# Performance work log

Hardware: AMD Instinct MI355X
Metric: run time of the kernel (lower is better)

The kernel has to match this reference:

```python
import jax, jax.numpy as jnp
import numpy as np

TEMPERATURE = 10.0
EPS = 1e-12  # torch F.normalize eps


def setup_inputs() -> dict:
    key = jax.random.key(0)
    k1, k2 = jax.random.split(key)
    B, D = 8192, 1024
    text_embeddings = jax.random.normal(k1, (B, D), dtype=jnp.float32)
    image_embeddings = jax.random.normal(k2, (B, D), dtype=jnp.float32)
    bias = jnp.zeros((1,), dtype=jnp.float32)
    return {
        "text_embeddings": text_embeddings,
        "image_embeddings": image_embeddings,
        "bias": bias,
    }


def _normalize(x):
    # matches torch F.normalize(p=2, dim=1): x / max(||x||, eps)
    norm = jnp.linalg.norm(x, axis=-1, keepdims=True)
    return x / jnp.maximum(norm, EPS)


def reference(text_embeddings, image_embeddings, bias):
    B = text_embeddings.shape[0]
    img_n = _normalize(image_embeddings)   # [B, D]
    txt_n = _normalize(text_embeddings)    # [B, D]
    # similarity[i, j] = <img_i, txt_j>
    sim = jnp.einsum('id,jd->ij', img_n, txt_n)          # [B, B]
    logits = sim * (-TEMPERATURE) + bias[0]
    labels = 2.0 * jnp.eye(B, dtype=logits.dtype) - 1.0   # +1 diag, -1 off-diag
    # loss_ij = log(1/(1+exp(label*logit))) = -softplus(label*logit)
    total_loss = -jnp.sum(jax.nn.softplus(labels * logits))
    return -(total_loss / B)
```

## Files before the change

### kernel.cpp

```cpp
#include <hip/hip_runtime.h>
#include <stdint.h>
#include <stddef.h>

#define NROWS 8192
#define DIM   1024
#define RB    512
#define TEMP  10.0f

#define BM 256
#define BN 256
#define BK 128

typedef __attribute__((ext_vector_type(8))) int i32x8;
typedef __attribute__((ext_vector_type(16))) float floatx16;

__device__ __forceinline__ void load16_lds(const unsigned char* g, unsigned char* l) {
    __builtin_amdgcn_global_load_lds(
        (__attribute__((address_space(1))) void*)(g),
        (__attribute__((address_space(3))) void*)(l),
        16, 0, 0);
}

__device__ __forceinline__ unsigned fp4q(float x) {
    float a = fabsf(x);
    a = fminf(a, 6.0f);
    unsigned c = (unsigned)(a >= 0.25f) + (unsigned)(a >= 0.75f)
               + (unsigned)(a >= 1.25f) + (unsigned)(a >= 1.75f)
               + (unsigned)(a >= 2.5f)  + (unsigned)(a >= 3.5f)
               + (unsigned)(a >= 5.0f);
    return c | ((__float_as_uint(x) >> 28) & 8u);
}

__device__ __forceinline__ i32x8 op8(int4 lo) {
    union { i32x8 v; int4 q[2]; } u;
    u.q[0] = lo;
    u.q[1] = make_int4(0, 0, 0, 0);
    return u.v;
}

__global__ __launch_bounds__(256) void normalize_kernel(
    const float* __restrict__ img, const float* __restrict__ txt,
    unsigned char* __restrict__ imgq, unsigned char* __restrict__ txtq,
    float* __restrict__ out)
{
    const int gw = blockIdx.x * 4 + (threadIdx.x >> 6);
    const int lane = threadIdx.x & 63;
    const float* src;
    unsigned char* dst;
    if (gw < NROWS) {
        src = img + (size_t)gw * DIM;
        dst = imgq + (size_t)gw * RB;
    } else {
        src = txt + (size_t)(gw - NROWS) * DIM;
        dst = txtq + (size_t)(gw - NROWS) * RB;
    }
    float4 v[4];
    float ss = 0.f;
#pragma unroll
    for (int c = 0; c < 4; c++) {
        v[c] = ((const float4*)src)[lane + 64 * c];
        ss += v[c].x * v[c].x + v[c].y * v[c].y + v[c].z * v[c].z + v[c].w * v[c].w;
    }
#pragma unroll
    for (int off = 32; off; off >>= 1) ss += __shfl_xor(ss, off);
    const float scale = 32.0f / fmaxf(sqrtf(ss), 1e-12f);
#pragma unroll
    for (int c = 0; c < 4; c++) {
        unsigned p = fp4q(v[c].x * scale)
                   | (fp4q(v[c].y * scale) << 4)
                   | (fp4q(v[c].z * scale) << 8)
                   | (fp4q(v[c].w * scale) << 12);
        ((unsigned short*)dst)[lane + 64 * c] = (unsigned short)p;
    }
    if (gw == 0 && lane == 0) out[0] = 0.f;
}

__global__ __launch_bounds__(512, 1) void simloss_kernel(
    const unsigned char* __restrict__ An,
    const unsigned char* __restrict__ Bn,
    const float* __restrict__ bias,
    float* __restrict__ out)
{
    __shared__ unsigned char As[2][BM * 64];
    __shared__ unsigned char Bs[2][BN * 64];
    __shared__ float red[24];

    const int t = threadIdx.x;
    const int lane = t & 63;
    const int wave = t >> 6;

    const int bid = blockIdx.x;
    const int blockN = (bid & 7) + 8 * ((bid >> 3) & 3);
    const int blockM = bid >> 5;

    int rowS[2], chS[2];
#pragma unroll
    for (int i = 0; i < 2; i++) {
        const int S = t + i * 512;
        const int pair = S >> 3, s7 = S & 7;
        rowS[i] = 2 * pair + (s7 & 1);
        chS[i] = ((s7 >> 1) ^ pair) & 3;
    }
    const unsigned char* gA0 = An + (size_t)(blockM * BM + rowS[0]) * RB + chS[0] * 16;
    const unsigned char* gA1 = An + (size_t)(blockM * BM + rowS[1]) * RB + chS[1] * 16;
    const unsigned char* gB0 = Bn + (size_t)(blockN * BN + rowS[0]) * RB + chS[0] * 16;
    const unsigned char* gB1 = Bn + (size_t)(blockN * BN + rowS[1]) * RB + chS[1] * 16;

    const int waveM = (wave >> 2) * 128;
    const int waveN = (wave & 3) * 64;
    const int fr = lane & 31;
    const int fh = lane >> 5;
    const int qk = (fr >> 1) & 3;
    const int po = 128 * (fr >> 1) + 16 * (fr & 1);
    const int offc0 = 32 * ((fh ^ qk) & 3);

    floatx16 acc[4][2];
#pragma unroll
    for (int mi = 0; mi < 4; mi++)
#pragma unroll
        for (int ni = 0; ni < 2; ni++)
            acc[mi][ni] = (floatx16)(0.f);

    load16_lds(gA0, &As[0][t * 16]);
    load16_lds(gA1, &As[0][t * 16 + 8192]);
    load16_lds(gB0, &Bs[0][t * 16]);
    load16_lds(gB1, &Bs[0][t * 16 + 8192]);

#pragma unroll
    for (int it = 0; it < DIM / BK; it++) {
        const int cur = it & 1;
        __syncthreads();
        if (it < DIM / BK - 1) {
            const int kb = (it + 1) * 64;
            load16_lds(gA0 + kb, &As[cur ^ 1][t * 16]);
            load16_lds(gA1 + kb, &As[cur ^ 1][t * 16 + 8192]);
            load16_lds(gB0 + kb, &Bs[cur ^ 1][t * 16]);
            load16_lds(gB1 + kb, &Bs[cur ^ 1][t * 16 + 8192]);
        }

        asm volatile("s_setprio 1");
#pragma unroll
        for (int ks = 0; ks < 2; ks++) {
            const int offc = offc0 ^ (ks << 6);
            int4 b[2];
#pragma unroll
            for (int ni = 0; ni < 2; ni++)
                b[ni] = *(const int4*)&Bs[cur][64 * (waveN + 32 * ni) + po + offc];
#pragma unroll
            for (int mi = 0; mi < 4; mi++) {
                int4 a = *(const int4*)&As[cur][64 * (waveM + 32 * mi) + po + offc];
#pragma unroll
                for (int ni = 0; ni < 2; ni++)
                    acc[mi][ni] = __builtin_amdgcn_mfma_scale_f32_32x32x64_f8f6f4(
                        op8(a), op8(b[ni]), acc[mi][ni],
                        4, 4,
                        0, 0x7f7f7f7f,
                        0, 0x7f7f7f7f);
            }
        }
        asm volatile("s_setprio 0");
    }

    const float bv = bias[0];
    const float c1 = -TEMP * 1.4426950408889634f / 1024.0f;
    const float c0 = bv * 1.4426950408889634f;
    float accP = 0.f, accQ = 0.f, accD = 0.f;
    const int gi0 = blockM * BM + waveM + 4 * fh;
    const int gj0 = blockN * BN + waveN + fr;
#pragma unroll
    for (int mi = 0; mi < 4; mi++) {
#pragma unroll
        for (int ni = 0; ni < 2; ni++) {
#pragma unroll
            for (int reg = 0; reg < 16; reg++) {
                float s = acc[mi][ni][reg];
                float w = fmaf(s, c1, c0);
                float e2 = __builtin_amdgcn_exp2f(-fabsf(w));
                accP += __builtin_amdgcn_logf(1.0f + e2);
                accP = fmaf(0.5f, fabsf(w), accP);
                accQ += s;
            }
        }
    }
    const bool diagblk = (blockN == blockM);
    if (diagblk) {
#pragma unroll
        for (int mi = 0; mi < 4; mi++)
#pragma unroll
            for (int ni = 0; ni < 2; ni++)
#pragma unroll
                for (int reg = 0; reg < 16; reg++) {
                    int ig = gi0 + mi * 32 + (reg & 3) + 8 * (reg >> 2);
                    int jg = gj0 + ni * 32;
                    if (ig == jg) accD += acc[mi][ni][reg];
                }
    }
#pragma unroll
    for (int off = 32; off; off >>= 1) {
        accP += __shfl_xor(accP, off);
        accQ += __shfl_xor(accQ, off);
        accD += __shfl_xor(accD, off);
    }
    if (lane == 0) {
        red[wave * 3 + 0] = accP;
        red[wave * 3 + 1] = accQ;
        red[wave * 3 + 2] = accD;
    }
    __syncthreads();
    if (t == 0) {
        float P = 0.f, Q = 0.f, D = 0.f;
#pragma unroll
        for (int w = 0; w < 8; w++) {
            P += red[w * 3 + 0];
            Q += red[w * 3 + 1];
            D += red[w * 3 + 2];
        }
        Q *= (1.0f / 1024.0f);
        D *= (1.0f / 1024.0f);
        float contrib = fmaf(0.6931471805599453f, P, fmaf(5.0f, Q, -32768.0f * bv));
        if (diagblk) contrib += fmaf(-TEMP, D, 256.0f * bv);
        atomicAdd(out, contrib * (1.0f / 8192.0f));
    }
}

extern "C" void kernel_launch(void* const* d_in, const int* in_sizes, int n_in,
                              void* d_out, int out_size, void* d_ws, size_t ws_size,
                              hipStream_t stream) {
    const float* txt = (const float*)d_in[0];
    const float* img = (const float*)d_in[1];
    const float* bias = (const float*)d_in[2];
    float* out = (float*)d_out;

    unsigned char* imgq = (unsigned char*)d_ws;
    unsigned char* txtq = imgq + (size_t)NROWS * RB;

    normalize_kernel<<<dim3(2 * NROWS / 4), dim3(256), 0, stream>>>(
        img, txt, imgq, txtq, out);

    simloss_kernel<<<dim3((NROWS / BM) * (NROWS / BN)), dim3(512), 0, stream>>>(
        imgq, txtq, bias, out);
}
```

Baseline: 152.6 us.

## Pre-tile quantized operands into MFMA fragment layout and triple-buffer LDS pipeline

The normalize kernel now stages quantized rows in shared memory and writes them in a tiled layout matching the MFMA fragment order, so the GEMM can load tiles with contiguous, swizzle-free addressing. The GEMM switches to a three-stage LDS ring with prefetch two iterations ahead, explicit vmcnt waits and raw barriers split per k-substep. Launch bounds are also relaxed to allow two blocks per CU. The aim is to hide global-to-LDS latency and simplify LDS reads. The cost is extra barriers, more shared memory per block (96KB), and a more intricate synchronisation scheme that must stay correct.

```diff
diff --git a/kernel.cpp b/kernel.cpp
--- a/kernel.cpp
+++ b/kernel.cpp
@@ -10,9 +10,13 @@
 #define BM 256
 #define BN 256
 #define BK 128
+#define NT (DIM / BK)
 
 typedef __attribute__((ext_vector_type(8))) int i32x8;
 typedef __attribute__((ext_vector_type(16))) float floatx16;
+
+#define FENCE() asm volatile("" ::: "memory")
+#define BARRIER() do { FENCE(); __builtin_amdgcn_s_barrier(); FENCE(); } while (0)
 
 __device__ __forceinline__ void load16_lds(const unsigned char* g, unsigned char* l) {
     __builtin_amdgcn_global_load_lds(
@@ -38,22 +42,18 @@
     return u.v;
 }
 
+
 __global__ __launch_bounds__(256) void normalize_kernel(
     const float* __restrict__ img, const float* __restrict__ txt,
     unsigned char* __restrict__ imgq, unsigned char* __restrict__ txtq,
     float* __restrict__ out)
 {
-    const int gw = blockIdx.x * 4 + (threadIdx.x >> 6);
-    const int lane = threadIdx.x & 63;
-    const float* src;
-    unsigned char* dst;
-    if (gw < NROWS) {
-        src = img + (size_t)gw * DIM;
-        dst = imgq + (size_t)gw * RB;
-    } else {
-        src = txt + (size_t)(gw - NROWS) * DIM;
-        dst = txtq + (size_t)(gw - NROWS) * RB;
-    }
+    __shared__ __align__(16) unsigned short sc[4][256];
+    const int t = threadIdx.x;
+    const int lane = t & 63, wave = t >> 6;
+    const int gw = blockIdx.x * 4 + wave;
+    const float* src = (gw < NROWS) ? img + (size_t)gw * DIM
+                                    : txt + (size_t)(gw - NROWS) * DIM;
     float4 v[4];
     float ss = 0.f;
 #pragma unroll
@@ -70,19 +70,29 @@
                    | (fp4q(v[c].y * scale) << 4)
                    | (fp4q(v[c].z * scale) << 8)
                    | (fp4q(v[c].w * scale) << 12);
-        ((unsigned short*)dst)[lane + 64 * c] = (unsigned short)p;
+        sc[wave][c * 64 + lane] = (unsigned short)p;
+    }
+    __syncthreads();
+    if (t < 128) {
+        const int rr = t & 3, k = t >> 2;
+        const int gr0 = blockIdx.x * 4;
+        unsigned char* dq = (gr0 < NROWS) ? imgq : txtq;
+        const int r = (gr0 < NROWS ? gr0 : gr0 - NROWS) + rr;
+        const int4 d = *(const int4*)&sc[rr][k * 8];
+        const int it = k >> 2, ks = (k >> 1) & 1, fh = k & 1;
+        *(int4*)(dq + (size_t)it * 524288 + (size_t)((r >> 5) * 2048
+                 + ks * 1024 + fh * 512 + (r & 31) * 16)) = d;
     }
     if (gw == 0 && lane == 0) out[0] = 0.f;
 }
 
-__global__ __launch_bounds__(512, 1) void simloss_kernel(
+__global__ __launch_bounds__(512, 2) void simloss_kernel(
     const unsigned char* __restrict__ An,
     const unsigned char* __restrict__ Bn,
     const float* __restrict__ bias,
     float* __restrict__ out)
 {
-    __shared__ unsigned char As[2][BM * 64];
-    __shared__ unsigned char Bs[2][BN * 64];
+    __shared__ __align__(16) unsigned char smem[3 * 32768];
     __shared__ float red[24];
 
     const int t = threadIdx.x;
@@ -93,26 +103,15 @@
     const int blockN = (bid & 7) + 8 * ((bid >> 3) & 3);
     const int blockM = bid >> 5;
 
-    int rowS[2], chS[2];
-#pragma unroll
-    for (int i = 0; i < 2; i++) {
-        const int S = t + i * 512;
-        const int pair = S >> 3, s7 = S & 7;
-        rowS[i] = 2 * pair + (s7 & 1);
-        chS[i] = ((s7 >> 1) ^ pair) & 3;
-    }
-    const unsigned char* gA0 = An + (size_t)(blockM * BM + rowS[0]) * RB + chS[0] * 16;
-    const unsigned char* gA1 = An + (size_t)(blockM * BM + rowS[1]) * RB + chS[1] * 16;
-    const unsigned char* gB0 = Bn + (size_t)(blockN * BN + rowS[0]) * RB + chS[0] * 16;
-    const unsigned char* gB1 = Bn + (size_t)(blockN * BN + rowS[1]) * RB + chS[1] * 16;
+    const unsigned char* gA = An + blockM * 16384 + t * 16;
+    const unsigned char* gB = Bn + blockN * 16384 + t * 16;
 
     const int waveM = (wave >> 2) * 128;
     const int waveN = (wave & 3) * 64;
+    const int rgA = (wave >> 2) * 4;
+    const int cgB = (wave & 3) * 2;
     const int fr = lane & 31;
     const int fh = lane >> 5;
-    const int qk = (fr >> 1) & 3;
-    const int po = 128 * (fr >> 1) + 16 * (fr & 1);
-    const int offc0 = 32 * ((fh ^ qk) & 3);
 
     floatx16 acc[4][2];
 #pragma unroll
@@ -121,44 +120,71 @@
         for (int ni = 0; ni < 2; ni++)
             acc[mi][ni] = (floatx16)(0.f);
 
-    load16_lds(gA0, &As[0][t * 16]);
-    load16_lds(gA1, &As[0][t * 16 + 8192]);
-    load16_lds(gB0, &Bs[0][t * 16]);
-    load16_lds(gB1, &Bs[0][t * 16 + 8192]);
-
-#pragma unroll
-    for (int it = 0; it < DIM / BK; it++) {
-        const int cur = it & 1;
-        __syncthreads();
-        if (it < DIM / BK - 1) {
-            const int kb = (it + 1) * 64;
-            load16_lds(gA0 + kb, &As[cur ^ 1][t * 16]);
-            load16_lds(gA1 + kb, &As[cur ^ 1][t * 16 + 8192]);
-            load16_lds(gB0 + kb, &Bs[cur ^ 1][t * 16]);
-            load16_lds(gB1 + kb, &Bs[cur ^ 1][t * 16 + 8192]);
-        }
-
-        asm volatile("s_setprio 1");
-#pragma unroll
-        for (int ks = 0; ks < 2; ks++) {
-            const int offc = offc0 ^ (ks << 6);
-            int4 b[2];
+    load16_lds(gA, smem + t * 16);
+    load16_lds(gA + 8192, smem + t * 16 + 8192);
+    load16_lds(gB, smem + 16384 + t * 16);
+    load16_lds(gB + 8192, smem + 16384 + t * 16 + 8192);
+    load16_lds(gA + 524288, smem + 32768 + t * 16);
+    load16_lds(gA + 524288 + 8192, smem + 32768 + t * 16 + 8192);
+    load16_lds(gB + 524288, smem + 32768 + 16384 + t * 16);
+    load16_lds(gB + 524288 + 8192, smem + 32768 + 16384 + t * 16 + 8192);
+    asm volatile("s_waitcnt vmcnt(4)" ::: "memory");
+    BARRIER();
+
+#pragma unroll
+    for (int it = 0; it < NT; ++it) {
+        const int buf = it % 3;
+        const int pbuf = (it + 2) % 3;
+        const unsigned char* Lw = smem + buf * 32768 + lane * 16;
+#pragma unroll
+        for (int ks = 0; ks < 2; ++ks) {
+            int4 aF[4], bF[2];
+#pragma unroll
+            for (int mi = 0; mi < 4; mi++)
+                aF[mi] = *(const int4*)(Lw + (rgA + mi) * 2048 + ks * 1024);
 #pragma unroll
             for (int ni = 0; ni < 2; ni++)
-                b[ni] = *(const int4*)&Bs[cur][64 * (waveN + 32 * ni) + po + offc];
-#pragma unroll
-            for (int mi = 0; mi < 4; mi++) {
-                int4 a = *(const int4*)&As[cur][64 * (waveM + 32 * mi) + po + offc];
+                bF[ni] = *(const int4*)(Lw + 16384 + (cgB + ni) * 2048 + ks * 1024);
+
+            if (it < NT - 2) {
+                const size_t ko = (size_t)(it + 2) * 524288;
+                unsigned char* Ld = smem + pbuf * 32768 + t * 16;
+                if (ks == 0) {
+                    load16_lds(gA + ko, Ld);
+                    load16_lds(gA + ko + 8192, Ld + 8192);
+                } else {
+                    load16_lds(gB + ko, Ld + 16384);
+                    load16_lds(gB + ko + 8192, Ld + 24576);
+                }
+            }
+            if (ks == 1) {
+                if (it < NT - 2) {
+                    asm volatile("s_waitcnt vmcnt(4)" ::: "memory");
+                } else if (it == NT - 2) {
+                    asm volatile("s_waitcnt vmcnt(0)" ::: "memory");
+                }
+            }
+            BARRIER();
+
+            i32x8 a8[4], b8[2];
+#pragma unroll
+            for (int mi = 0; mi < 4; mi++) a8[mi] = op8(aF[mi]);
+#pragma unroll
+            for (int ni = 0; ni < 2; ni++) b8[ni] = op8(bF[ni]);
+
+            asm volatile("s_setprio 1");
+#pragma unroll
+            for (int mi = 0; mi < 4; mi++)
 #pragma unroll
                 for (int ni = 0; ni < 2; ni++)
                     acc[mi][ni] = __builtin_amdgcn_mfma_scale_f32_32x32x64_f8f6f4(
-                        op8(a), op8(b[ni]), acc[mi][ni],
+                        a8[mi], b8[ni], acc[mi][ni],
                         4, 4,
                         0, 0x7f7f7f7f,
                         0, 0x7f7f7f7f);
-            }
+            asm volatile("s_setprio 0");
+            BARRIER();
         }
-        asm volatile("s_setprio 0");
     }
 
     const float bv = bias[0];
```

Result: faster. 142.6 us (-6.6%).
